# Performance work log

Measured on AMD Instinct MI355X. Metric: run time of the kernel, lower is better.

## Reference

```python
import jax, jax.numpy as jnp
import numpy as np

NUM_HEADS = 32


def setup_inputs() -> dict:
    key = jax.random.key(0)
    ks = jax.random.split(key, 6)
    B, S, D = 1, 2048, 4096
    hd = D // NUM_HEADS  # 128
    x = jax.random.normal(ks[0], (B, S, D), dtype=jnp.float32)
    # true rotary frequencies: freqs_cis = exp(i * t * theta^{-2j/hd})
    inv_freq = 1.0 / (10000.0 ** (jnp.arange(0, hd, 2, dtype=jnp.float32) / hd))  # [hd//2]
    angles = jnp.arange(S, dtype=jnp.float32)[:, None] * inv_freq[None, :]  # [S, hd//2]
    freqs_cos = jnp.cos(angles)
    freqs_sin = jnp.sin(angles)
    scale = 0.02
    wq = jax.random.normal(ks[1], (D, D), dtype=jnp.float32) * scale
    wk = jax.random.normal(ks[2], (D, D), dtype=jnp.float32) * scale
    wv = jax.random.normal(ks[3], (D, D), dtype=jnp.float32) * scale
    wo = jax.random.normal(ks[4], (D, D), dtype=jnp.float32) * scale
    return {"x": x, "freqs_cos": freqs_cos, "freqs_sin": freqs_sin,
            "wq": wq, "wk": wk, "wv": wv, "wo": wo}


def _apply_rope(t, cos, sin):
    # t: [B, S, H, hd]; cos/sin: [S, hd//2]
    B, S, H, hd = t.shape
    tr = t.reshape(B, S, H, hd // 2, 2)
    a, b = tr[..., 0], tr[..., 1]
    c = cos[None, :, None, :]
    s = sin[None, :, None, :]
    out_r = a * c - b * s
    out_i = a * s + b * c
    return jnp.stack([out_r, out_i], axis=-1).reshape(B, S, H, hd)


def reference(x, freqs_cos, freqs_sin, wq, wk, wv, wo):
    B, S, D = x.shape
    H = NUM_HEADS
    hd = D // H
    xq = (x @ wq).reshape(B, S, H, hd)
    xk = (x @ wk).reshape(B, S, H, hd)
    xv = (x @ wv).reshape(B, S, H, hd)
    xq = _apply_rope(xq, freqs_cos, freqs_sin)
    xk = _apply_rope(xk, freqs_cos, freqs_sin)
    # [B, H, S, hd]
    xq = xq.transpose(0, 2, 1, 3)
    xk = xk.transpose(0, 2, 1, 3)
    xv = xv.transpose(0, 2, 1, 3)
    scores = jnp.einsum('bhqd,bhkd->bhqk', xq, xk) / jnp.sqrt(jnp.float32(hd))
    scores = jax.nn.softmax(scores.astype(jnp.float32), axis=-1).astype(xq.dtype)
    out = jnp.einsum('bhqk,bhkd->bhqd', scores, xv)
    out = out.transpose(0, 2, 1, 3).reshape(B, S, D)
    return out @ wo
```

## Files before the change

kernel.cpp:

```cpp
#include <hip/hip_runtime.h>
#include <hip/hip_bf16.h>

typedef __hip_bfloat16 bf16;
typedef __attribute__((ext_vector_type(8))) short short8;
typedef __attribute__((ext_vector_type(4))) short short4v;
typedef __attribute__((ext_vector_type(4))) float f32x4;

#define MFMA16(a, b, c) __builtin_amdgcn_mfma_f32_16x16x32_bf16((a), (b), (c), 0, 0, 0)

static __device__ __forceinline__ void gload_lds16(const bf16* g, bf16* l) {
  __builtin_amdgcn_global_load_lds((const __attribute__((address_space(1))) unsigned int*)g,
                                   (__attribute__((address_space(3))) unsigned int*)l,
                                   16, 0, 0);
}

__global__ __launch_bounds__(256) void castx_kernel(const float* __restrict__ x,
                                                    bf16* __restrict__ xb, int n) {
  int i = (blockIdx.x * 256 + threadIdx.x) * 8;
  if (i >= n) return;
  float4 v0 = *(const float4*)(x + i);
  float4 v1 = *(const float4*)(x + i + 4);
  bf16 tmp[8];
  tmp[0] = __float2bfloat16(v0.x); tmp[1] = __float2bfloat16(v0.y);
  tmp[2] = __float2bfloat16(v0.z); tmp[3] = __float2bfloat16(v0.w);
  tmp[4] = __float2bfloat16(v1.x); tmp[5] = __float2bfloat16(v1.y);
  tmp[6] = __float2bfloat16(v1.z); tmp[7] = __float2bfloat16(v1.w);
  *(short8*)(xb + i) = *(short8*)tmp;
}

__global__ __launch_bounds__(256) void tw_kernel(const float* __restrict__ W,
                                                 bf16* __restrict__ WT) {
  __shared__ bf16 tile[64][65];
  int b = blockIdx.x;
  int tk = (b >> 6) * 64;
  int tn = (b & 63) * 64;
  int t = threadIdx.x;
  int c = t & 63, r0 = t >> 6;
#pragma unroll
  for (int i = 0; i < 16; ++i) {
    int r = i * 4 + r0;
    tile[c][r] = __float2bfloat16(W[(size_t)(tk + r) * 4096 + tn + c]);
  }
  __syncthreads();
#pragma unroll
  for (int i = 0; i < 16; ++i) {
    int r = i * 4 + r0;
    WT[(size_t)(tn + r) * 4096 + tk + c] = tile[r][c];
  }
}

__global__ __launch_bounds__(512) void gemmQK(const bf16* __restrict__ A,
                                              const bf16* __restrict__ Bt,
                                              bf16* __restrict__ Qb,
                                              bf16* __restrict__ Kb,
                                              const float* __restrict__ fcos,
                                              const float* __restrict__ fsin) {
  __shared__ bf16 LDS[3 * 16384];
  const int K = 4096, NK = 128;
  int g = blockIdx.x;
  int wid = (g & 7) * 32 + (g >> 3);
  int bm = wid >> 5, bn = wid & 31;
  int t = threadIdx.x, lane = t & 63, w = t >> 6;
  int wm = w >> 2, wn = w & 3;
  int lr = lane & 15, lg = lane >> 4;
  int rg = lg ^ ((lr >> 1) & 3);
  f32x4 acc[8][4] = {};

  const bf16* Ab = A + (size_t)bm * 256 * K;
  const bf16* Bb = Bt + (size_t)bn * 256 * K;
  int srow = t >> 2;
  int sg = (t & 3) ^ ((t >> 3) & 3);

#define STG(buf, kt2, mat, i)                                                     \
  gload_lds16(((mat) ? Bb : Ab) + (size_t)((i) * 128 + srow) * K + (kt2) * 32 + sg * 8, \
              LDS + (buf) * 16384 + (mat) * 8192 + (i) * 4096 + w * 512)
#define AFR(la, mi) \
  (*(const short8*)(LDS + (la) + (wm * 128 + (mi) * 16 + lr) * 32 + (rg << 3)))
#define BFR(la, nf) \
  (*(const short8*)(LDS + (la) + 8192 + (wn * 64 + (nf) * 16 + lr) * 32 + (rg << 3)))

  STG(0, 0, 0, 0); STG(0, 0, 0, 1); STG(0, 0, 1, 0); STG(0, 0, 1, 1);
  STG(1, 1, 0, 0); STG(1, 1, 0, 1); STG(1, 1, 1, 0); STG(1, 1, 1, 1);
  asm volatile("s_waitcnt vmcnt(4)" ::: "memory");
  __builtin_amdgcn_s_barrier();

  int cur = 0;
  for (int kt = 0; kt < NK; ++kt) {
    int la = cur * 16384;
    int stb = (cur + 2 >= 3) ? cur - 1 : cur + 2;
    bool pf = (kt + 2) < NK;
    short8 b[4], a0, a1;

    b[0] = BFR(la, 0); b[1] = BFR(la, 1); b[2] = BFR(la, 2); b[3] = BFR(la, 3);
    a0 = AFR(la, 0); a1 = AFR(la, 1);
    if (pf) STG(stb, kt + 2, 0, 0);
    __builtin_amdgcn_s_barrier();
    __builtin_amdgcn_s_setprio(1);
#pragma unroll
    for (int nf = 0; nf < 4; ++nf) {
      acc[0][nf] = MFMA16(a0, b[nf], acc[0][nf]);
      acc[1][nf] = MFMA16(a1, b[nf], acc[1][nf]);
    }
    __builtin_amdgcn_s_setprio(0);
    __builtin_amdgcn_s_barrier();

    a0 = AFR(la, 2); a1 = AFR(la, 3);
    if (pf) STG(stb, kt + 2, 0, 1);
    __builtin_amdgcn_s_barrier();
    __builtin_amdgcn_s_setprio(1);
#pragma unroll
    for (int nf = 0; nf < 4; ++nf) {
      acc[2][nf] = MFMA16(a0, b[nf], acc[2][nf]);
      acc[3][nf] = MFMA16(a1, b[nf], acc[3][nf]);
    }
    __builtin_amdgcn_s_setprio(0);
    __builtin_amdgcn_s_barrier();

    a0 = AFR(la, 4); a1 = AFR(la, 5);
    if (pf) STG(stb, kt + 2, 1, 0);
    __builtin_amdgcn_s_barrier();
    __builtin_amdgcn_s_setprio(1);
#pragma unroll
    for (int nf = 0; nf < 4; ++nf) {
      acc[4][nf] = MFMA16(a0, b[nf], acc[4][nf]);
      acc[5][nf] = MFMA16(a1, b[nf], acc[5][nf]);
    }
    __builtin_amdgcn_s_setprio(0);
    __builtin_amdgcn_s_barrier();

    a0 = AFR(la, 6); a1 = AFR(la, 7);
    if (pf) STG(stb, kt + 2, 1, 1);
    __builtin_amdgcn_s_barrier();
    __builtin_amdgcn_s_setprio(1);
#pragma unroll
    for (int nf = 0; nf < 4; ++nf) {
      acc[6][nf] = MFMA16(a0, b[nf], acc[6][nf]);
      acc[7][nf] = MFMA16(a1, b[nf], acc[7][nf]);
    }
    __builtin_amdgcn_s_setprio(0);
    if (pf)
      asm volatile("s_waitcnt vmcnt(4)" ::: "memory");
    else
      asm volatile("s_waitcnt vmcnt(0)" ::: "memory");
    __builtin_amdgcn_s_barrier();

    cur = (cur + 1 == 3) ? 0 : cur + 1;
  }
#undef STG
#undef AFR
#undef BFR

  int sect = bn >> 4, bnl = bn & 15;
  bf16* Cb = sect ? Kb : Qb;
  const float qs = sect ? 1.0f : 0.08838834764831845f;
#pragma unroll
  for (int mi = 0; mi < 8; ++mi)
#pragma unroll
    for (int nf = 0; nf < 4; ++nf) {
      int col = bnl * 256 + wn * 64 + nf * 16 + lr;
      int row0 = bm * 256 + wm * 128 + mi * 16 + lg * 4;
      int ip = (col >> 1) & 63;
      float sgn = (col & 1) ? 1.0f : -1.0f;
#pragma unroll
      for (int r = 0; r < 4; ++r) {
        int row = row0 + r;
        float mine = acc[mi][nf][r];
        float oth = __shfl_xor(mine, 1);
        float cv = fcos[row * 64 + ip];
        float sv = fsin[row * 64 + ip];
        float v = (mine * cv + sgn * oth * sv) * qs;
        Cb[(size_t)row * 4096 + col] = __float2bfloat16(v);
      }
    }
}

template <int EPI>
__global__ __launch_bounds__(512) void gemm4(const bf16* __restrict__ A,
                                             const bf16* __restrict__ Bt,
                                             void* __restrict__ Cv,
                                             int M, int N, int K) {
  __shared__ bf16 LDS[3][384 * 64];
  const int NB = N >> 8;
  int g = blockIdx.x;
  int nwg = (M >> 7) * NB;
  int wid = (g & 7) * (nwg >> 3) + (g >> 3);
  int bm = wid / NB, bn = wid % NB;
  int t = threadIdx.x, lane = t & 63, w = t >> 6;
  int wm = w >> 2, wn = w & 3;
  int lr = lane & 15, lg = lane >> 4;
  int rsw = lr & 7;
  f32x4 acc[4][4] = {};

  const bf16* Ab = A + (size_t)bm * 128 * K;
  const bf16* Bb = Bt + (size_t)bn * 256 * K;
  int srow = t >> 3;
  int sg = (t & 7) ^ (srow & 7);
  int NK = K >> 6;

#define STA(buf, kt2, i)                                                        \
  gload_lds16(Ab + (size_t)((i) * 64 + srow) * K + (kt2) * 64 + sg * 8,         \
              LDS[buf] + ((i) * 512 + w * 64) * 8)
#define STB(buf, kt2, i)                                                        \
  gload_lds16(Bb + (size_t)((i) * 64 + srow) * K + (kt2) * 64 + sg * 8,         \
              LDS[buf] + 128 * 64 + ((i) * 512 + w * 64) * 8)
#define AFRAG(la, m, kc) \
  (*(const short8*)((la) + (wm * 64 + (m) * 16 + lr) * 64 + ((((kc) * 4 + lg) ^ rsw) << 3)))
#define BFRAG(lb, nf, kc) \
  (*(const short8*)((lb) + (wn * 64 + (nf) * 16 + lr) * 64 + ((((kc) * 4 + lg) ^ rsw) << 3)))

  STA(0, 0, 0); STA(0, 0, 1);
  STB(0, 0, 0); STB(0, 0, 1); STB(0, 0, 2); STB(0, 0, 3);
  STA(1, 1, 0); STA(1, 1, 1);
  STB(1, 1, 0); STB(1, 1, 1); STB(1, 1, 2); STB(1, 1, 3);
  asm volatile("s_waitcnt vmcnt(6)" ::: "memory");
  __builtin_amdgcn_s_barrier();

  int cur = 0;
  for (int kt = 0; kt < NK; ++kt) {
    const bf16* la = LDS[cur];
    const bf16* lb = la + 128 * 64;
    int nb2 = cur + 2; if (nb2 >= 3) nb2 -= 3;
    bool pf = (kt + 2) < NK;
    short8 a0[2][2], a1[2][2], b0[2][2], b1[2][2];

#pragma unroll
    for (int i = 0; i < 2; ++i)
#pragma unroll
      for (int kc = 0; kc < 2; ++kc) {
        a0[i][kc] = AFRAG(la, i, kc);
        b0[i][kc] = BFRAG(lb, i, kc);
      }
    if (pf) { STA(nb2, kt + 2, 0); STA(nb2, kt + 2, 1); }
    __builtin_amdgcn_s_barrier();
    __builtin_amdgcn_s_setprio(1);
#pragma unroll
    for (int i = 0; i < 2; ++i)
#pragma unroll
      for (int j = 0; j < 2; ++j)
#pragma unroll
        for (int kc = 0; kc < 2; ++kc)
          acc[i][j] = MFMA16(a0[i][kc], b0[j][kc], acc[i][j]);
    __builtin_amdgcn_s_setprio(0);
    __builtin_amdgcn_s_barrier();

#pragma unroll
    for (int j = 0; j < 2; ++j)
#pragma unroll
      for (int kc = 0; kc < 2; ++kc)
        b1[j][kc] = BFRAG(lb, 2 + j, kc);
    if (pf) { STB(nb2, kt + 2, 0); STB(nb2, kt + 2, 1); }
    __builtin_amdgcn_s_barrier();
    __builtin_amdgcn_s_setprio(1);
#pragma unroll
    for (int i = 0; i < 2; ++i)
#pragma unroll
      for (int j = 0; j < 2; ++j)
#pragma unroll
        for (int kc = 0; kc < 2; ++kc)
          acc[i][2 + j] = MFMA16(a0[i][kc], b1[j][kc], acc[i][2 + j]);
    __builtin_amdgcn_s_setprio(0);
    __builtin_amdgcn_s_barrier();

#pragma unroll
    for (int i = 0; i < 2; ++i)
#pragma unroll
      for (int kc = 0; kc < 2; ++kc)
        a1[i][kc] = AFRAG(la, 2 + i, kc);
    if (pf) { STB(nb2, kt + 2, 2); STB(nb2, kt + 2, 3); }
    __builtin_amdgcn_s_barrier();
    __builtin_amdgcn_s_setprio(1);
#pragma unroll
    for (int i = 0; i < 2; ++i)
#pragma unroll
      for (int j = 0; j < 2; ++j)
#pragma unroll
        for (int kc = 0; kc < 2; ++kc)
          acc[2 + i][j] = MFMA16(a1[i][kc], b0[j][kc], acc[2 + i][j]);
    __builtin_amdgcn_s_setprio(0);
    __builtin_amdgcn_s_barrier();

    __builtin_amdgcn_s_setprio(1);
#pragma unroll
    for (int i = 0; i < 2; ++i)
#pragma unroll
      for (int j = 0; j < 2; ++j)
#pragma unroll
        for (int kc = 0; kc < 2; ++kc)
          acc[2 + i][2 + j] = MFMA16(a1[i][kc], b1[j][kc], acc[2 + i][2 + j]);
    __builtin_amdgcn_s_setprio(0);
    if (pf)
      asm volatile("s_waitcnt vmcnt(6)" ::: "memory");
    else
      asm volatile("s_waitcnt vmcnt(0)" ::: "memory");
    __builtin_amdgcn_s_barrier();

    cur = (cur + 1 == 3) ? 0 : cur + 1;
  }
#undef STA
#undef STB
#undef AFRAG
#undef BFRAG

#pragma unroll
  for (int m = 0; m < 4; ++m)
#pragma unroll
    for (int nf = 0; nf < 4; ++nf) {
      int col = bn * 256 + wn * 64 + nf * 16 + lr;
      int row0 = bm * 128 + wm * 64 + m * 16 + lg * 4;
      if constexpr (EPI == 3) {
        bf16 tmp[4];
#pragma unroll
        for (int r = 0; r < 4; ++r) tmp[r] = __float2bfloat16(acc[m][nf][r]);
        *(short4v*)((bf16*)Cv + (size_t)col * M + row0) = *(short4v*)tmp;
      } else {
#pragma unroll
        for (int r = 0; r < 4; ++r) {
          int row = row0 + r;
          ((float*)Cv)[(size_t)row * N + col] = acc[m][nf][r];
        }
      }
    }
}

__global__ __launch_bounds__(512, 2) void attn_fwd(const bf16* __restrict__ Q,
                                                   const bf16* __restrict__ K,
                                                   const bf16* __restrict__ Vt,
                                                   bf16* __restrict__ O) {
  __shared__ bf16 Kbuf[2][64 * 128];
  __shared__ bf16 Vbuf[2][128 * 64];
  __shared__ char Ps_all[8][2][2048];
  const int S = 2048, D = 4096, HD = 128, NT = 32;
  int g = blockIdx.y * 8 + blockIdx.x;
  int wid = (g & 7) * 32 + (g >> 3);
  int h = wid >> 3, qb = wid & 7;
  int tid = threadIdx.x, lane = tid & 63, w = tid >> 6;
  int lr = lane & 15, lg = lane >> 4;
  int q0 = qb * 256 + w * 32;
  int swz = (lr & 7) << 4;

  const bf16* Kh = K + h * HD;
  const bf16* Vh = Vt + (size_t)h * HD * S;

  short8 aq[2][4];
#pragma unroll
  for (int u = 0; u < 2; ++u)
#pragma unroll
    for (int c = 0; c < 4; ++c)
      aq[u][c] = *(const short8*)(Q + (size_t)(q0 + u * 16 + lr) * D + h * HD + c * 32 + lg * 8);

  int kr = lane >> 4, ksl = lane & 15;
  int vr = lane >> 3, vsl = lane & 7;

  f32x4 accO[2][8] = {};
  float lsum[2] = {0.f, 0.f};

#define STAGE(b, ttile)                                                            \
  do {                                                                             \
    int kv0_ = (ttile) * 64;                                                       \
    _Pragma("unroll") for (int ii = 0; ii < 2; ++ii) {                             \
      int row = w * 8 + ii * 4 + kr;                                               \
      gload_lds16(Kh + (size_t)(kv0_ + row) * D + ((ksl ^ (row & 7)) << 3),        \
                  &Kbuf[b][(w * 8 + ii * 4) * 128]);                               \
    }                                                                              \
    _Pragma("unroll") for (int ii = 0; ii < 2; ++ii) {                             \
      int row = w * 16 + ii * 8 + vr;                                              \
      gload_lds16(Vh + (size_t)row * S + kv0_ + ((vsl ^ (row & 7)) << 3),          \
                  &Vbuf[b][(w * 16 + ii * 8) * 64]);                               \
    }                                                                              \
  } while (0)

  int cur = 0;
  STAGE(0, 0);
  for (int tt = 0; tt < NT; ++tt) {
    if (tt + 1 < NT) {
      STAGE(cur ^ 1, tt + 1);
      asm volatile("s_waitcnt vmcnt(4)" ::: "memory");
    } else {
      asm volatile("s_waitcnt vmcnt(0)" ::: "memory");
    }
    __builtin_amdgcn_s_barrier();
    const bf16* Kb_ = Kbuf[cur];
    const bf16* Vb_ = Vbuf[cur];

    f32x4 sf[2][4] = {};
#pragma unroll
    for (int j = 0; j < 4; ++j)
#pragma unroll
      for (int c = 0; c < 4; ++c) {
        short8 kf = *(const short8*)(Kb_ + (j * 16 + lr) * 128 +
                                     (((c * 4 + lg) ^ (lr & 7)) << 3));
        sf[0][j] = MFMA16(kf, aq[0][c], sf[0][j]);
        sf[1][j] = MFMA16(kf, aq[1][c], sf[1][j]);
      }
#pragma unroll
    for (int u = 0; u < 2; ++u) {
      char* Ps = Ps_all[w][u];
#pragma unroll
      for (int j = 0; j < 4; ++j) {
        float p0 = __expf(sf[u][j][0]);
        float p1 = __expf(sf[u][j][1]);
        float p2 = __expf(sf[u][j][2]);
        float p3 = __expf(sf[u][j][3]);
        lsum[u] += (p0 + p1) + (p2 + p3);
        bf16 pk[4] = {__float2bfloat16(p0), __float2bfloat16(p1),
                      __float2bfloat16(p2), __float2bfloat16(p3)};
        *(short4v*)(Ps + lr * 128 + ((j * 32 + lg * 8) ^ swz)) = *(short4v*)pk;
      }
    }
#pragma unroll
    for (int t2 = 0; t2 < 2; ++t2) {
      short8 pa0 = *(const short8*)(Ps_all[w][0] + lr * 128 + ((t2 * 64 + lg * 16) ^ swz));
      short8 pa1 = *(const short8*)(Ps_all[w][1] + lr * 128 + ((t2 * 64 + lg * 16) ^ swz));
#pragma unroll
      for (int n = 0; n < 8; ++n) {
        short8 bv = *(const short8*)(Vb_ + (n * 16 + lr) * 64 +
                                     (((t2 * 4 + lg) ^ (lr & 7)) << 3));
        accO[0][n] = MFMA16(pa0, bv, accO[0][n]);
        accO[1][n] = MFMA16(pa1, bv, accO[1][n]);
      }
    }
    __builtin_amdgcn_s_barrier();
    cur ^= 1;
  }
#undef STAGE

#pragma unroll
  for (int u = 0; u < 2; ++u) {
    float ls = lsum[u];
    ls += __shfl_xor(ls, 16);
    ls += __shfl_xor(ls, 32);
    float rs[4];
#pragma unroll
    for (int r = 0; r < 4; ++r)
      rs[r] = 1.f / __shfl(ls, lg * 4 + r);
#pragma unroll
    for (int n = 0; n < 8; ++n)
#pragma unroll
      for (int r = 0; r < 4; ++r) {
        int row = q0 + u * 16 + lg * 4 + r;
        int col = h * HD + n * 16 + lr;
        O[(size_t)row * D + col] = __float2bfloat16(accO[u][n][r] * rs[r]);
      }
  }
}

extern "C" void kernel_launch(void* const* d_in, const int* in_sizes, int n_in,
                              void* d_out, int out_size, void* d_ws, size_t ws_size,
                              hipStream_t stream) {
  const float* x    = (const float*)d_in[0];
  const float* fcos = (const float*)d_in[1];
  const float* fsin = (const float*)d_in[2];
  const float* wq   = (const float*)d_in[3];
  const float* wk   = (const float*)d_in[4];
  const float* wv   = (const float*)d_in[5];
  const float* wo   = (const float*)d_in[6];
  float* out = (float*)d_out;

  const int S = 2048, D = 4096;
  const size_t MB = 1024 * 1024;
  char* ws = (char*)d_ws;
  bf16* xb  = (bf16*)(ws);
  bf16* wT2 = (bf16*)(ws + 16 * MB);
  bf16* Vt  = (bf16*)(ws + 48 * MB);
  bf16* Qb  = (bf16*)(ws + 80 * MB);
  bf16* Kb  = (bf16*)(ws + 96 * MB);
  bf16* AO  = (bf16*)(ws);

  int n = S * D;
  castx_kernel<<<n / (256 * 8), 256, 0, stream>>>(x, xb, n);

  tw_kernel<<<4096, 256, 0, stream>>>(wq, wT2);
  tw_kernel<<<4096, 256, 0, stream>>>(wk, wT2 + (size_t)4096 * 4096);
  gemmQK<<<256, 512, 0, stream>>>(xb, wT2, Qb, Kb, fcos, fsin);

  tw_kernel<<<4096, 256, 0, stream>>>(wv, wT2);
  gemm4<3><<<256, 512, 0, stream>>>(xb, wT2, Vt, S, D, D);

  attn_fwd<<<dim3(8, 32), 512, 0, stream>>>(Qb, Kb, Vt, AO);

  tw_kernel<<<4096, 256, 0, stream>>>(wo, wT2);
  gemm4<4><<<256, 512, 0, stream>>>(AO, wT2, out, S, D, D);
}
```

Measured before the change: 428.3 us.

## Restructure QK GEMM to double-buffered K=64 tiles with XCD-aware block mapping

The fused Q/K projection GEMM moves from a triple-buffered pipeline with 32-wide K steps to a double-buffered one with 64-wide K steps (two 32-wide halves per buffer). This halves the number of outer iterations and issues MFMAs in larger 4x4 groups per phase. It also changes the block-to-tile mapping so that each XCD works on a 4x8 rectangle of output tiles, which should improve L2 reuse of A and B. The cost is a larger LDS footprint and prefetch depth dropping from two stages to one, which could expose more memory latency.

```diff
diff --git a/kernel.cpp b/kernel.cpp
--- a/kernel.cpp
+++ b/kernel.cpp
@@ -49,94 +49,82 @@
   }
 }
 
-__global__ __launch_bounds__(512) void gemmQK(const bf16* __restrict__ A,
-                                              const bf16* __restrict__ Bt,
-                                              bf16* __restrict__ Qb,
-                                              bf16* __restrict__ Kb,
-                                              const float* __restrict__ fcos,
-                                              const float* __restrict__ fsin) {
-  __shared__ bf16 LDS[3 * 16384];
-  const int K = 4096, NK = 128;
+__global__ __launch_bounds__(512) void gemmQK8(const bf16* __restrict__ A,
+                                               const bf16* __restrict__ Bt,
+                                               bf16* __restrict__ Qb,
+                                               bf16* __restrict__ Kb,
+                                               const float* __restrict__ fcos,
+                                               const float* __restrict__ fsin) {
+  __shared__ bf16 LDS[2 * 32768];
+  const int K = 4096, NK = 64;
   int g = blockIdx.x;
-  int wid = (g & 7) * 32 + (g >> 3);
-  int bm = wid >> 5, bn = wid & 31;
+  int xcd = g & 7, loc = g >> 3;
+  int bm = (xcd >> 2) * 4 + (loc >> 3);
+  int bn = (xcd & 3) * 8 + (loc & 7);
   int t = threadIdx.x, lane = t & 63, w = t >> 6;
   int wm = w >> 2, wn = w & 3;
   int lr = lane & 15, lg = lane >> 4;
-  int rg = lg ^ ((lr >> 1) & 3);
+  int rsw = (lr >> 1) & 3;
   f32x4 acc[8][4] = {};
 
   const bf16* Ab = A + (size_t)bm * 256 * K;
   const bf16* Bb = Bt + (size_t)bn * 256 * K;
-  int srow = t >> 2;
+  int sr4 = t >> 2;
   int sg = (t & 3) ^ ((t >> 3) & 3);
 
-#define STG(buf, kt2, mat, i)                                                     \
-  gload_lds16(((mat) ? Bb : Ab) + (size_t)((i) * 128 + srow) * K + (kt2) * 32 + sg * 8, \
-              LDS + (buf) * 16384 + (mat) * 8192 + (i) * 4096 + w * 512)
-#define AFR(la, mi) \
-  (*(const short8*)(LDS + (la) + (wm * 128 + (mi) * 16 + lr) * 32 + (rg << 3)))
-#define BFR(la, nf) \
-  (*(const short8*)(LDS + (la) + 8192 + (wn * 64 + (nf) * 16 + lr) * 32 + (rg << 3)))
-
-  STG(0, 0, 0, 0); STG(0, 0, 0, 1); STG(0, 0, 1, 0); STG(0, 0, 1, 1);
-  STG(1, 1, 0, 0); STG(1, 1, 0, 1); STG(1, 1, 1, 0); STG(1, 1, 1, 1);
+#define SA(nb, kt2, kh)                                                          \
+  do {                                                                           \
+    _Pragma("unroll") for (int j = 0; j < 2; ++j)                                \
+      gload_lds16(Ab + (size_t)(j * 128 + sr4) * K + (kt2) * 64 + (kh) * 32 + sg * 8, \
+                  LDS + (nb) + (kh) * 8192 + (j * 512 + t) * 8);                 \
+  } while (0)
+#define SB(nb, kt2, kh)                                                          \
+  do {                                                                           \
+    _Pragma("unroll") for (int j = 0; j < 2; ++j)                                \
+      gload_lds16(Bb + (size_t)(j * 128 + sr4) * K + (kt2) * 64 + (kh) * 32 + sg * 8, \
+                  LDS + (nb) + 16384 + (kh) * 8192 + (j * 512 + t) * 8);         \
+  } while (0)
+#define AFR(base, kc, mi) \
+  (*(const short8*)(LDS + (base) + (kc) * 8192 + (wm * 128 + (mi) * 16 + lr) * 32 + ((lg ^ rsw) << 3)))
+#define BFR(base, kc, nf) \
+  (*(const short8*)(LDS + (base) + 16384 + (kc) * 8192 + (wn * 64 + (nf) * 16 + lr) * 32 + ((lg ^ rsw) << 3)))
+
+  SA(0, 0, 0); SB(0, 0, 0); SA(0, 0, 1); SB(0, 0, 1);
   asm volatile("s_waitcnt vmcnt(4)" ::: "memory");
   __builtin_amdgcn_s_barrier();
 
   int cur = 0;
   for (int kt = 0; kt < NK; ++kt) {
-    int la = cur * 16384;
-    int stb = (cur + 2 >= 3) ? cur - 1 : cur + 2;
-    bool pf = (kt + 2) < NK;
-    short8 b[4], a0, a1;
-
-    b[0] = BFR(la, 0); b[1] = BFR(la, 1); b[2] = BFR(la, 2); b[3] = BFR(la, 3);
-    a0 = AFR(la, 0); a1 = AFR(la, 1);
-    if (pf) STG(stb, kt + 2, 0, 0);
-    __builtin_amdgcn_s_barrier();
-    __builtin_amdgcn_s_setprio(1);
-#pragma unroll
-    for (int nf = 0; nf < 4; ++nf) {
-      acc[0][nf] = MFMA16(a0, b[nf], acc[0][nf]);
-      acc[1][nf] = MFMA16(a1, b[nf], acc[1][nf]);
-    }
-    __builtin_amdgcn_s_setprio(0);
-    __builtin_amdgcn_s_barrier();
-
-    a0 = AFR(la, 2); a1 = AFR(la, 3);
-    if (pf) STG(stb, kt + 2, 0, 1);
-    __builtin_amdgcn_s_barrier();
-    __builtin_amdgcn_s_setprio(1);
-#pragma unroll
-    for (int nf = 0; nf < 4; ++nf) {
-      acc[2][nf] = MFMA16(a0, b[nf], acc[2][nf]);
-      acc[3][nf] = MFMA16(a1, b[nf], acc[3][nf]);
-    }
-    __builtin_amdgcn_s_setprio(0);
-    __builtin_amdgcn_s_barrier();
-
-    a0 = AFR(la, 4); a1 = AFR(la, 5);
-    if (pf) STG(stb, kt + 2, 1, 0);
-    __builtin_amdgcn_s_barrier();
-    __builtin_amdgcn_s_setprio(1);
-#pragma unroll
-    for (int nf = 0; nf < 4; ++nf) {
-      acc[4][nf] = MFMA16(a0, b[nf], acc[4][nf]);
-      acc[5][nf] = MFMA16(a1, b[nf], acc[5][nf]);
-    }
-    __builtin_amdgcn_s_setprio(0);
-    __builtin_amdgcn_s_barrier();
-
-    a0 = AFR(la, 6); a1 = AFR(la, 7);
-    if (pf) STG(stb, kt + 2, 1, 1);
-    __builtin_amdgcn_s_barrier();
-    __builtin_amdgcn_s_setprio(1);
-#pragma unroll
-    for (int nf = 0; nf < 4; ++nf) {
-      acc[6][nf] = MFMA16(a0, b[nf], acc[6][nf]);
-      acc[7][nf] = MFMA16(a1, b[nf], acc[7][nf]);
-    }
+    int base = cur * 32768;
+    int nbf = (cur ^ 1) * 32768;
+    bool pf = (kt + 1) < NK;
+    short8 a[4], b[4];
+
+#pragma unroll
+    for (int nf = 0; nf < 4; ++nf) b[nf] = BFR(base, 0, nf);
+#pragma unroll
+    for (int i = 0; i < 4; ++i) a[i] = AFR(base, 0, i);
+    if (pf) SA(nbf, kt + 1, 0);
+    __builtin_amdgcn_s_barrier();
+    __builtin_amdgcn_s_setprio(1);
+#pragma unroll
+    for (int i = 0; i < 4; ++i)
+#pragma unroll
+      for (int nf = 0; nf < 4; ++nf)
+        acc[i][nf] = MFMA16(a[i], b[nf], acc[i][nf]);
+    __builtin_amdgcn_s_setprio(0);
+    __builtin_amdgcn_s_barrier();
+
+#pragma unroll
+    for (int i = 0; i < 4; ++i) a[i] = AFR(base, 0, 4 + i);
+    if (pf) SB(nbf, kt + 1, 0);
+    __builtin_amdgcn_s_barrier();
+    __builtin_amdgcn_s_setprio(1);
+#pragma unroll
+    for (int i = 0; i < 4; ++i)
+#pragma unroll
+      for (int nf = 0; nf < 4; ++nf)
+        acc[4 + i][nf] = MFMA16(a[i], b[nf], acc[4 + i][nf]);
     __builtin_amdgcn_s_setprio(0);
     if (pf)
       asm volatile("s_waitcnt vmcnt(4)" ::: "memory");
@@ -144,9 +132,39 @@
       asm volatile("s_waitcnt vmcnt(0)" ::: "memory");
     __builtin_amdgcn_s_barrier();
 
-    cur = (cur + 1 == 3) ? 0 : cur + 1;
+#pragma unroll
+    for (int nf = 0; nf < 4; ++nf) b[nf] = BFR(base, 1, nf);
+#pragma unroll
+    for (int i = 0; i < 4; ++i) a[i] = AFR(base, 1, i);
+    if (pf) SA(nbf, kt + 1, 1);
+    __builtin_amdgcn_s_barrier();
+    __builtin_amdgcn_s_setprio(1);
+#pragma unroll
+    for (int i = 0; i < 4; ++i)
+#pragma unroll
+      for (int nf = 0; nf < 4; ++nf)
+        acc[i][nf] = MFMA16(a[i], b[nf], acc[i][nf]);
+    __builtin_amdgcn_s_setprio(0);
+    __builtin_amdgcn_s_barrier();
+
+#pragma unroll
+    for (int i = 0; i < 4; ++i) a[i] = AFR(base, 1, 4 + i);
+    if (pf) SB(nbf, kt + 1, 1);
+    __builtin_amdgcn_s_barrier();
+    __builtin_amdgcn_s_setprio(1);
+#pragma unroll
+    for (int i = 0; i < 4; ++i)
+#pragma unroll
+      for (int nf = 0; nf < 4; ++nf)
+        acc[4 + i][nf] = MFMA16(a[i], b[nf], acc[4 + i][nf]);
+    __builtin_amdgcn_s_setprio(0);
+    asm volatile("s_waitcnt vmcnt(4)" ::: "memory");
+    __builtin_amdgcn_s_barrier();
+
+    cur ^= 1;
   }
-#undef STG
+#undef SA
+#undef SB
 #undef AFR
 #undef BFR
 
@@ -471,7 +489,7 @@
 
   tw_kernel<<<4096, 256, 0, stream>>>(wq, wT2);
   tw_kernel<<<4096, 256, 0, stream>>>(wk, wT2 + (size_t)4096 * 4096);
-  gemmQK<<<256, 512, 0, stream>>>(xb, wT2, Qb, Kb, fcos, fsin);
+  gemmQK8<<<256, 512, 0, stream>>>(xb, wT2, Qb, Kb, fcos, fsin);
 
   tw_kernel<<<4096, 256, 0, stream>>>(wv, wT2);
   gemm4<3><<<256, 512, 0, stream>>>(xb, wT2, Vt, S, D, D);
```

After: 419.0 us. 2.2% less time.
